# Kernel tuning notes

Hardware: AMD Instinct MI355X
Metric: run time of the kernel (lower is better)

## Reference

```python
import jax, jax.numpy as jnp
import numpy as np

NEG_INF = jnp.float32(-2**32 + 1)  # matches the module's padding constant


def setup_inputs() -> dict:
    key = jax.random.key(0)
    ks = jax.random.split(key, 20)
    T, N, E, R = 4, 20000, 320000, 2
    Din, Dh, H = 64, 64, 4
    s = 0.1  # xavier-ish scale
    inp = {
        "x": jax.random.normal(ks[0], (T, N, Din), jnp.float32),
        "edge_index": jax.random.randint(ks[1], (T, R, 2, E), 0, N, jnp.int32),
        "W_src": jax.random.normal(ks[2], (R, Din, H * Dh), jnp.float32) * s,
        "W_dst": jax.random.normal(ks[3], (R, Din, H * Dh), jnp.float32) * s,
        "att_src": jax.random.normal(ks[4], (R, H, Dh), jnp.float32) * s,
        "att_dst": jax.random.normal(ks[5], (R, H, Dh), jnp.float32) * s,
        "ra_W1": jax.random.normal(ks[6], (Dh, 4 * Dh), jnp.float32) * s,
        "ra_b1": jnp.zeros((4 * Dh,), jnp.float32),
        "ra_W2": jax.random.normal(ks[7], (4 * Dh, 1), jnp.float32) * s,
        "lstm_Wih": jax.random.normal(ks[8], (4 * Dh, Dh), jnp.float32) * s,
        "lstm_Whh": jax.random.normal(ks[9], (4 * Dh, Dh), jnp.float32) * s,
        "lstm_bih": jnp.zeros((4 * Dh,), jnp.float32),
        "lstm_bhh": jnp.zeros((4 * Dh,), jnp.float32),
        "pos_emb": jax.random.normal(ks[10], (T, Dh), jnp.float32) * s,
        "Wq": jax.random.normal(ks[11], (Dh, Dh), jnp.float32) * s,
        "Wk": jax.random.normal(ks[12], (Dh, Dh), jnp.float32) * s,
        "Wv": jax.random.normal(ks[13], (Dh, Dh), jnp.float32) * s,
    }
    return inp


def _gat(xt, ei, Ws, Wd, a_s, a_d, N, H, C):
    # PyG GATConv, concat=False, bias=False, eval mode (no dropout)
    src, dst = ei[0], ei[1]
    hs = (xt @ Ws).reshape(N, H, C)
    hd = (xt @ Wd).reshape(N, H, C)
    als = (hs * a_s[None]).sum(-1)          # [N,H]
    ald = (hd * a_d[None]).sum(-1)          # [N,H]
    e = jax.nn.leaky_relu(als[src] + ald[dst], 0.2)   # [E,H]
    m = jax.ops.segment_max(e, dst, num_segments=N)   # [N,H]
    p = jnp.exp(e - m[dst])
    denom = jax.ops.segment_sum(p, dst, num_segments=N)
    alpha = p / (denom[dst] + 1e-16)
    out = jax.ops.segment_sum(hs[src] * alpha[:, :, None], dst, num_segments=N)  # [N,H,C]
    return out.mean(1)                      # concat=False -> mean over heads


def reference(x, edge_index, W_src, W_dst, att_src, att_dst,
              ra_W1, ra_b1, ra_W2,
              lstm_Wih, lstm_Whh, lstm_bih, lstm_bhh,
              pos_emb, Wq, Wk, Wv):
    T, N, _ = x.shape
    R, H, C = att_src.shape   # C == n_hid (per-head GAT channels)

    # ---- intra-relation aggregation: GATConv per etype, vmapped over timeframes
    intra = []
    for r in range(R):
        f = jax.vmap(lambda xt, ei, r=r: _gat(xt, ei, W_src[r], W_dst[r],
                                              att_src[r], att_dst[r], N, H, C))
        intra.append(f(x, edge_index[:, r]))      # [T,N,C]
    h = jnp.stack(intra, axis=2)                  # [T,N,R,C]

    # ---- inter-relation aggregation (RelationAgg), batched over timeframes
    s = jnp.tanh(h @ ra_W1 + ra_b1) @ ra_W2       # [T,N,R,1]
    beta = jax.nn.softmax(s.mean(1), axis=1)      # mean over nodes, softmax over R -> [T,R,1]
    inter = (beta[:, None] * h).sum(2)            # [T,N,C]

    # ---- LSTM over time (batch = nodes)
    def step(carry, xt):
        hh, cc = carry
        g = xt @ lstm_Wih.T + hh @ lstm_Whh.T + lstm_bih + lstm_bhh
        i, f_, gg, o = jnp.split(g, 4, axis=-1)   # torch gate order i,f,g,o
        cc = jax.nn.sigmoid(f_) * cc + jax.nn.sigmoid(i) * jnp.tanh(gg)
        hh = jax.nn.sigmoid(o) * jnp.tanh(cc)
        return (hh, cc), hh
    z = jnp.zeros((N, C), x.dtype)
    _, hs_seq = jax.lax.scan(step, (z, z), inter)  # [T,N,C]
    feats = hs_seq.transpose(1, 0, 2)              # [N,T,C]

    # ---- temporal multi-head attention with causal mask, eval mode
    Ch = C // H
    ti = feats + pos_emb[None]                     # positions are just arange(T)
    qh = (ti @ Wq).reshape(N, T, H, Ch)
    kh = (ti @ Wk).reshape(N, T, H, Ch)
    vh = (ti @ Wv).reshape(N, T, H, Ch)
    scores = jnp.einsum('nqhc,nkhc->nhqk', qh, kh) / jnp.sqrt(jnp.float32(T))
    mask = jnp.tril(jnp.ones((T, T), bool))
    scores = jnp.where(mask[None, None], scores, NEG_INF)
    a = jax.nn.softmax(scores, axis=-1)
    out = jnp.einsum('nhqk,nkhc->nqhc', a, vh).reshape(N, T, C)
    return out  # output_features[ttype][ntype] == out[:, i, :]
```

## Files before the change

### kernel.cpp

```cpp
#include <hip/hip_runtime.h>
#include <hip/hip_bf16.h>

#define T_ 4
#define N_ 20000
#define E_ 320000
#define R_ 2
#define DIN 64
#define G_ 256
#define P_ 8
#define BPAD 18432
#define NB_ 32
#define EPB_ 10000
#define CHN_ 625

typedef unsigned short u16;
typedef __attribute__((ext_vector_type(8))) short bf16x8;
typedef __attribute__((ext_vector_type(2))) _Float16 h2;
typedef __attribute__((ext_vector_type(4))) float f32x4;

__device__ __forceinline__ float bf2f(u16 u) {
    unsigned int i = ((unsigned int)u) << 16; float f;
    __builtin_memcpy(&f, &i, 4); return f;
}
__device__ __forceinline__ u16 f2bf(float f) {
    unsigned int i; __builtin_memcpy(&i, &f, 4);
    unsigned int r = i + 0x7fffu + ((i >> 16) & 1u);
    return (u16)(r >> 16);
}
__device__ __forceinline__ u16 f2h(float f) {
    union { _Float16 h; u16 u; } c; c.h = (_Float16)f; return c.u;
}
__device__ __forceinline__ float sigm(float x) { return 1.f / (1.f + __expf(-x)); }
__device__ __forceinline__ float ftanh(float x) { return 1.f - 2.f / (__expf(2.f * x) + 1.f); }
__device__ __forceinline__ float fdot2(h2 a, h2 b, float c) {
#if __has_builtin(__builtin_amdgcn_fdot2)
    return __builtin_amdgcn_fdot2(a, b, c, false);
#else
    float r;
    asm("v_dot2_f32_f16 %0, %1, %2, %3" : "=v"(r) : "v"(a), "v"(b), "v"(c));
    return r;
#endif
}

__device__ __forceinline__ void gemm_direct(
    const u16* __restrict__ A, const u16* __restrict__ Bpad,
    int M, int Astride, int kchunks, int m0, f32x4* acc)
{
    const int tid = threadIdx.x;
    const int lane = tid & 63, wv = tid >> 6;
    const int col = lane & 15, quad = lane >> 4;
    #pragma unroll
    for (int cf = 0; cf < 16; ++cf) { acc[cf][0]=0.f; acc[cf][1]=0.f; acc[cf][2]=0.f; acc[cf][3]=0.f; }

    int row = m0 + wv * 16 + col;
    int row_c = (row < M) ? row : (M - 1);

    for (int kc = 0; kc < kchunks; ++kc) {
        #pragma unroll
        for (int ks = 0; ks < 2; ++ks) {
            bf16x8 a = *(const bf16x8*)(A + (size_t)row_c * Astride + kc * 64 + ks * 32 + quad * 8);
            const u16* bb = Bpad + kc * BPAD + ks * 32 + quad * 8;
            #pragma unroll
            for (int cf = 0; cf < 16; ++cf) {
                bf16x8 b = *(const bf16x8*)(bb + (cf * 16 + col) * 72);
                acc[cf] = __builtin_amdgcn_mfma_f32_16x16x32_bf16(a, b, acc[cf], 0, 0, 0);
            }
        }
    }
}

__global__ __launch_bounds__(256) void k_fold(
    const float* __restrict__ x, const float* __restrict__ wdall,
    float* __restrict__ als_all, float* __restrict__ ald_all, u16* __restrict__ x_h)
{
    __shared__ float wds[1024];
    {
        int tid = threadIdx.x;
        *(float4*)(wds + tid * 4) = *(const float4*)(wdall + tid * 4);
    }
    __syncthreads();

    int t = blockIdx.y;
    int idx = blockIdx.x * 256 + threadIdx.x;
    if (idx >= N_ * 4) return;
    int n = idx >> 2, q = idx & 3;
    const float* xr = x + ((size_t)t * N_ + n) * 64 + q * 16;
    float4 xv[4];
    #pragma unroll
    for (int i = 0; i < 4; ++i) xv[i] = *(const float4*)(xr + i * 4);

    {
        union { u16 h[16]; ushort4 s4[4]; } cv;
        #pragma unroll
        for (int i = 0; i < 4; ++i) {
            cv.h[i*4+0] = f2h(xv[i].x); cv.h[i*4+1] = f2h(xv[i].y);
            cv.h[i*4+2] = f2h(xv[i].z); cv.h[i*4+3] = f2h(xv[i].w);
        }
        u16* xo = x_h + ((size_t)t * N_ + n) * 64 + q * 16;
        #pragma unroll
        for (int i = 0; i < 4; ++i) *(ushort4*)(xo + i * 4) = cv.s4[i];
    }

    float s[16];
    #pragma unroll
    for (int i = 0; i < 16; ++i) s[i] = 0.f;
    #pragma unroll
    for (int i = 0; i < 4; ++i) {
        float xe[4] = {xv[i].x, xv[i].y, xv[i].z, xv[i].w};
        #pragma unroll
        for (int e = 0; e < 4; ++e) {
            int k = q * 16 + i * 4 + e;
            float xk = xe[e];
            #pragma unroll
            for (int tb = 0; tb < 4; ++tb) {
                float4 w = *(const float4*)(wds + tb * 256 + k * 4);
                s[tb*4+0] += xk * w.x; s[tb*4+1] += xk * w.y;
                s[tb*4+2] += xk * w.z; s[tb*4+3] += xk * w.w;
            }
        }
    }
    #pragma unroll
    for (int i = 0; i < 16; ++i) {
        s[i] += __shfl_xor(s[i], 1);
        s[i] += __shfl_xor(s[i], 2);
    }
    if (q == 0) {
        *(float4*)(als_all + ((size_t)(t*2+0) * N_ + n) * 4) = make_float4(s[0], s[1], s[2], s[3]);
        *(float4*)(als_all + ((size_t)(t*2+1) * N_ + n) * 4) = make_float4(s[4], s[5], s[6], s[7]);
        *(float4*)(ald_all + ((size_t)(t*2+0) * N_ + n) * 4) = make_float4(s[8], s[9], s[10], s[11]);
        *(float4*)(ald_all + ((size_t)(t*2+1) * N_ + n) * 4) = make_float4(s[12], s[13], s[14], s[15]);
    }
}

__global__ void k_prep(const float* __restrict__ Wdst, const float* __restrict__ att_dst,
                       const float* __restrict__ Wih, const float* __restrict__ Whh,
                       const float* __restrict__ bih, const float* __restrict__ bhh,
                       const float* __restrict__ Wsrc, const float* __restrict__ att_src,
                       const float* __restrict__ raW1,
                       const float* __restrict__ Wq, const float* __restrict__ Wk,
                       const float* __restrict__ Wv,
                       float* __restrict__ wdall, float* __restrict__ biasv,
                       u16* __restrict__ raW1_pad, u16* __restrict__ Wc_pad,
                       u16* __restrict__ qkv_pad, u16* __restrict__ postB_pad)
{
    int tid = threadIdx.x, bid = blockIdx.x;
    if (bid == 0) {
        int k = tid >> 2, h = tid & 3;
        for (int r = 0; r < 2; ++r) {
            float ss = 0.f, sd = 0.f;
            for (int c = 0; c < 64; ++c) {
                ss += Wsrc[((size_t)r * 64 + k) * 256 + h * 64 + c] * att_src[r * 256 + h * 64 + c];
                sd += Wdst[((size_t)r * 64 + k) * 256 + h * 64 + c] * att_dst[r * 256 + h * 64 + c];
            }
            wdall[r * 256 + k * 4 + h] = ss;
            wdall[512 + r * 256 + k * 4 + h] = sd;
        }
        biasv[tid] = bih[tid] + bhh[tid];
    }
    for (int i = bid * 256 + tid; i < BPAD; i += gridDim.x * 256) {
        int n = i / 72, kk = i % 72;
        raW1_pad[i] = (kk < 64) ? f2bf(raW1[kk * 256 + n]) : (u16)0;
    }
    for (int i = bid * 256 + tid; i < 2 * BPAD; i += gridDim.x * 256) {
        int kc = i / BPAD, q = i % BPAD, n = q / 72, kk = q % 72;
        const float* W = kc ? Whh : Wih;
        Wc_pad[i] = (kk < 64) ? f2bf(W[n * 64 + kk]) : (u16)0;
    }
    for (int i = bid * 256 + tid; i < 192 * 72; i += gridDim.x * 256) {
        int g = i / 72, kk = i % 72;
        int j = g >> 6, c = g & 63;
        const float* W = (j == 0) ? Wq : (j == 1) ? Wk : Wv;
        qkv_pad[i] = (kk < 64) ? f2bf(W[kk * 64 + c]) : (u16)0;
    }
    for (int i = bid * 256 + tid; i < 2 * 4 * 4608; i += gridDim.x * 256) {
        int r = i / 18432, q = i % 18432, kc = q / 4608, qq = q % 4608;
        int c = qq / 72, kk = qq % 72;
        postB_pad[i] = (kk < 64) ? f2bf(Wsrc[(size_t)r * 16384 + kk * 256 + kc * 64 + c]) : (u16)0;
    }
}

__global__ __launch_bounds__(256) void k_hist(const int* __restrict__ ei,
                                              u16* __restrict__ rank, u16* __restrict__ partial)
{
    __shared__ unsigned int hist[N_ / 2];
    int b = blockIdx.x, p = blockIdx.y, tid = threadIdx.x;
    for (int i = tid; i < N_ / 2; i += 256) hist[i] = 0u;
    __syncthreads();
    const int* dsts = ei + ((size_t)p * 2 + 1) * E_ + b * EPB_;
    u16* rk = rank + (size_t)p * E_ + b * EPB_;
    for (int e = tid; e < EPB_; e += 256) {
        int dst = dsts[e];
        unsigned sh = (unsigned)(dst & 1) * 16u;
        unsigned old = atomicAdd(&hist[dst >> 1], 1u << sh);
        rk[e] = (u16)((old >> sh) & 0xffffu);
    }
    __syncthreads();
    u16* part = partial + ((size_t)p * NB_ + b) * N_;
    for (int n = tid; n < N_; n += 256) {
        unsigned hv = hist[n >> 1];
        part[n] = (u16)((hv >> ((unsigned)(n & 1) * 16u)) & 0xffffu);
    }
}

__global__ __launch_bounds__(256) void k_scan1(u16* __restrict__ partial,
                                               int* __restrict__ offsets, int* __restrict__ chunktot)
{
    int p = blockIdx.y, ch = blockIdx.x;
    int tid = threadIdx.x, lane = tid & 63, wid = tid >> 6;
    __shared__ int wtot[4];
    u16* part = partial + (size_t)p * NB_ * N_;
    int* ofs = offsets + (size_t)p * (N_ + 1);
    int n0 = ch * CHN_;
    int carry = 0;
    for (int rnd = 0; rnd < 3; ++rnd) {
        int i = rnd * 256 + tid;
        int n = n0 + i;
        int v = 0;
        if (i < CHN_) {
            int run = 0;
            #pragma unroll 8
            for (int b = 0; b < NB_; ++b) {
                int pv = part[b * N_ + n];
                part[b * N_ + n] = (u16)run;
                run += pv;
            }
            v = run;
        }
        int incl = v;
        for (int d = 1; d < 64; d <<= 1) { int u = __shfl_up(incl, d); if (lane >= d) incl += u; }
        if (lane == 63) wtot[wid] = incl;
        __syncthreads();
        if (tid < 4) {
            int iv = wtot[tid];
            for (int d = 1; d < 4; d <<= 1) { int u = __shfl_up(iv, d); if (tid >= d) iv += u; }
            wtot[tid] = iv;
        }
        __syncthreads();
        int woff = (wid > 0) ? wtot[wid - 1] : 0;
        int tot = wtot[3];
        int excl = carry + woff + incl - v;
        if (i < CHN_) ofs[n] = excl;
        carry += tot;
        __syncthreads();
    }
    if (tid == 0) chunktot[p * NB_ + ch] = carry;
}

__global__ void k_scan2(const int* __restrict__ chunktot, int* __restrict__ chunkbase) {
    int tid = threadIdx.x;
    if (tid < P_) {
        int run = 0;
        for (int c = 0; c < NB_; ++c) {
            chunkbase[tid * NB_ + c] = run;
            run += chunktot[tid * NB_ + c];
        }
    }
}

__global__ void k_scan3(int* __restrict__ offsets, const int* __restrict__ chunkbase) {
    int p = blockIdx.y;
    int n = blockIdx.x * 256 + threadIdx.x;
    if (n < N_)
        offsets[(size_t)p * (N_ + 1) + n] += chunkbase[p * NB_ + n / CHN_];
    if (n == 0)
        offsets[(size_t)p * (N_ + 1) + N_] = E_;
}

__global__ void k_scatter(const int* __restrict__ ei, const int* __restrict__ offsets,
                          const u16* __restrict__ rank, const u16* __restrict__ partial,
                          u16* __restrict__ csr) {
    int bid = blockIdx.x;
    int p = bid & 7;
    int e = (bid >> 3) * 256 + threadIdx.x;
    int src = ei[((size_t)p * 2 + 0) * E_ + e];
    int dst = ei[((size_t)p * 2 + 1) * E_ + e];
    int b = e / EPB_;
    int pos = offsets[p * (N_ + 1) + dst]
            + (int)partial[((size_t)p * NB_ + b) * N_ + dst]
            + (int)rank[(size_t)p * E_ + e];
    csr[(size_t)p * E_ + pos] = (u16)src;
}

__global__ __launch_bounds__(256) void k_agg(
    const int* __restrict__ offsets, const u16* __restrict__ csr,
    const float* __restrict__ als_all, const float* __restrict__ ald_all,
    const u16* __restrict__ x_h, u16* __restrict__ xagg4)
{
    __shared__ __align__(16) u16 ptab[4][256];
    const int bid = blockIdx.x;
    const int p = bid & 7;
    const int t = p >> 1;
    const int* off   = offsets + (size_t)p * (N_ + 1);
    const u16* srcs  = csr + (size_t)p * E_;
    const float* als = als_all + (size_t)p * N_ * 4;
    const float* ald = ald_all + (size_t)p * N_ * 4;
    const u16* xb    = x_h + (size_t)t * N_ * 64;

    const int tid = threadIdx.x, lane = tid & 63, wv = tid >> 6;
    const int n = (bid >> 3) * 4 + wv;
    const int o0 = off[n], o1 = off[n + 1];
    const float4 aldv = *(const float4*)(ald + (size_t)n * 4);
    u16* pt = &ptab[wv][0];
    const int pw = (lane >> 1) * 8 + (lane & 1);

    float a0 = 0.f, a1 = 0.f, a2 = 0.f, a3 = 0.f;
    float d0 = 0.f, d1 = 0.f, d2 = 0.f, d3 = 0.f;

    for (int base = o0; base < o1; base += 64) {
        int cnt = o1 - base; if (cnt > 64) cnt = 64;
        int sv = 0;
        float p0 = 0.f, p1 = 0.f, p2 = 0.f, p3 = 0.f;
        if (lane < cnt) {
            sv = (int)srcs[base + lane];
            float4 av = *(const float4*)(als + (size_t)sv * 4);
            float e0 = av.x + aldv.x, e1 = av.y + aldv.y;
            float e2 = av.z + aldv.z, e3 = av.w + aldv.w;
            e0 = (e0 > 0.f) ? e0 : 0.2f * e0;
            e1 = (e1 > 0.f) ? e1 : 0.2f * e1;
            e2 = (e2 > 0.f) ? e2 : 0.2f * e2;
            e3 = (e3 > 0.f) ? e3 : 0.2f * e3;
            p0 = __expf(e0); p1 = __expf(e1); p2 = __expf(e2); p3 = __expf(e3);
        }
        d0 += p0; d1 += p1; d2 += p2; d3 += p3;
        pt[pw + 0] = f2h(p0); pt[pw + 2] = f2h(p1);
        pt[pw + 4] = f2h(p2); pt[pw + 6] = f2h(p3);
        int cntR = __builtin_amdgcn_readfirstlane((cnt + 7) & ~7);
        for (int j0 = 0; j0 < cntR; j0 += 8) {
            #pragma unroll
            for (int pr = 0; pr < 4; ++pr) {
                int j = j0 + pr * 2;
                int s0 = __builtin_amdgcn_readlane(sv, j);
                int s1 = __builtin_amdgcn_readlane(sv, j + 1);
                unsigned x0 = xb[((size_t)(unsigned)s0 << 6) + lane];
                unsigned x1 = xb[((size_t)(unsigned)s1 << 6) + lane];
                unsigned xp = x0 | (x1 << 16);
                uint4 pp = *(const uint4*)(pt + (j >> 1) * 8);
                h2 xv, q0, q1, q2, q3;
                __builtin_memcpy(&xv, &xp, 4);
                __builtin_memcpy(&q0, &pp.x, 4);
                __builtin_memcpy(&q1, &pp.y, 4);
                __builtin_memcpy(&q2, &pp.z, 4);
                __builtin_memcpy(&q3, &pp.w, 4);
                a0 = fdot2(xv, q0, a0);
                a1 = fdot2(xv, q1, a1);
                a2 = fdot2(xv, q2, a2);
                a3 = fdot2(xv, q3, a3);
            }
        }
    }
    #pragma unroll
    for (int m = 1; m < 64; m <<= 1) {
        d0 += __shfl_xor(d0, m); d1 += __shfl_xor(d1, m);
        d2 += __shfl_xor(d2, m); d3 += __shfl_xor(d3, m);
    }
    float s0 = 0.25f / (d0 + 1e-16f), s1 = 0.25f / (d1 + 1e-16f);
    float s2 = 0.25f / (d2 + 1e-16f), s3 = 0.25f / (d3 + 1e-16f);
    u16* outp = xagg4 + ((size_t)p * N_ + n) * 256 + lane;
    outp[0]   = f2bf(a0 * s0);
    outp[64]  = f2bf(a1 * s1);
    outp[128] = f2bf(a2 * s2);
    outp[192] = f2bf(a3 * s3);
}

__global__ __launch_bounds__(256) void k_post(
    const u16* __restrict__ xagg4, const u16* __restrict__ postB_pad,
    u16* __restrict__ intra)
{
    const int t = blockIdx.z, r = blockIdx.y;
    const u16* A = xagg4 + ((size_t)(t * 2 + r)) * N_ * 256;
    const u16* Bp = postB_pad + (size_t)r * 4 * 4608;
    const int tid = threadIdx.x, lane = tid & 63, wv = tid >> 6;
    const int col = lane & 15, quad = lane >> 4;
    int m0 = blockIdx.x * 64;
    int row = m0 + wv * 16 + col;
    int row_c = (row < N_) ? row : (N_ - 1);

    f32x4 acc[4];
    #pragma unroll
    for (int cf = 0; cf < 4; ++cf) { acc[cf][0]=0.f; acc[cf][1]=0.f; acc[cf][2]=0.f; acc[cf][3]=0.f; }
    #pragma unroll
    for (int kc = 0; kc < 4; ++kc) {
        #pragma unroll
        for (int ks = 0; ks < 2; ++ks) {
            bf16x8 a = *(const bf16x8*)(A + (size_t)row_c * 256 + kc * 64 + ks * 32 + quad * 8);
            const u16* bb = Bp + kc * 4608 + ks * 32 + quad * 8;
            #pragma unroll
            for (int cf = 0; cf < 4; ++cf) {
                bf16x8 b = *(const bf16x8*)(bb + (cf * 16 + col) * 72);
                acc[cf] = __builtin_amdgcn_mfma_f32_16x16x32_bf16(a, b, acc[cf], 0, 0, 0);
            }
        }
    }
    int rowbase = m0 + wv * 16 + quad * 4;
    #pragma unroll
    for (int cf = 0; cf < 4; ++cf) {
        int c = cf * 16 + col;
        #pragma unroll
        for (int reg = 0; reg < 4; ++reg) {
            int rr = rowbase + reg;
            if (rr < N_)
                intra[(((size_t)t * N_ + rr) * 2 + r) * 64 + c] = f2bf(acc[cf][reg]);
        }
    }
}

__global__ __launch_bounds__(256) void k_relagg(
    const u16* __restrict__ A, const u16* __restrict__ W1pad, const float* __restrict__ b1,
    const float* __restrict__ W2, float* __restrict__ ssum)
{
    int m0 = blockIdx.x * 64;
    f32x4 acc[16];
    gemm_direct(A, W1pad, T_ * N_ * R_, 64, 1, m0, acc);

    const int tid = threadIdx.x, lane = tid & 63, wv = tid >> 6;
    const int col = lane & 15;
    float sp[4] = {0.f, 0.f, 0.f, 0.f};
    #pragma unroll
    for (int cf = 0; cf < 16; ++cf) {
        int gcol = cf * 16 + col;
        float bb = b1[gcol];
        float ww = W2[gcol];
        #pragma unroll
        for (int reg = 0; reg < 4; ++reg)
            sp[reg] += ftanh(acc[cf][reg] + bb) * ww;
    }
    #pragma unroll
    for (int reg = 0; reg < 4; ++reg) {
        float v = sp[reg];
        v += __shfl_xor(v, 1); v += __shfl_xor(v, 2);
        v += __shfl_xor(v, 4); v += __shfl_xor(v, 8);
        sp[reg] = v;
    }
    float se = sp[0] + sp[2];
    float so = sp[1] + sp[3];
    se += __shfl_xor(se, 16); se += __shfl_xor(se, 32);
    so += __shfl_xor(so, 16); so += __shfl_xor(so, 32);
    __shared__ float red[8];
    if (lane == 0) { red[wv * 2] = se; red[wv * 2 + 1] = so; }
    __syncthreads();
    if (tid == 0) {
        float s0 = red[0] + red[2] + red[4] + red[6];
        float s1 = red[1] + red[3] + red[5] + red[7];
        int t = m0 / (N_ * R_);
        atomicAdd(&ssum[t * 2 + 0], s0);
        atomicAdd(&ssum[t * 2 + 1], s1);
    }
}

__global__ __launch_bounds__(256) void k_lstm(
    const u16* __restrict__ intra, const float* __restrict__ ssum,
    const u16* __restrict__ Wc_pad, const float* __restrict__ biasv,
    u16* __restrict__ feats)
{
    __shared__ __align__(16) u16 hl[64][72];
    const int tid = threadIdx.x, lane = tid & 63, wv = tid >> 6;
    const int col = lane & 15, quad = lane >> 4;
    int m0 = blockIdx.x * 64;
    int row = m0 + wv * 16 + col;
    int row_c = (row < N_) ? row : (N_ - 1);
    int rowbase = m0 + wv * 16 + quad * 4;

    float betas[8];
    #pragma unroll
    for (int t = 0; t < 4; ++t) {
        float s0 = ssum[t * 2] * (1.f / N_), s1 = ssum[t * 2 + 1] * (1.f / N_);
        float mx = fmaxf(s0, s1);
        float e0 = __expf(s0 - mx), e1 = __expf(s1 - mx);
        float inv = 1.f / (e0 + e1);
        betas[t * 2] = e0 * inv; betas[t * 2 + 1] = e1 * inv;
    }

    float cc[4][4];
    #pragma unroll
    for (int j = 0; j < 4; ++j)
        #pragma unroll
        for (int reg = 0; reg < 4; ++reg) cc[j][reg] = 0.f;

    for (int t = 0; t < 4; ++t) {
        float b0 = betas[t * 2], b1 = betas[t * 2 + 1];
        const u16* ib = intra + ((size_t)t * N_ + row_c) * 128;

        f32x4 acc[16];
        #pragma unroll
        for (int cf = 0; cf < 16; ++cf) { acc[cf][0]=0.f; acc[cf][1]=0.f; acc[cf][2]=0.f; acc[cf][3]=0.f; }

        #pragma unroll
        for (int ks = 0; ks < 2; ++ks) {
            int coff = ks * 32 + quad * 8;
            bf16x8 i0 = *(const bf16x8*)(ib + coff);
            bf16x8 i1 = *(const bf16x8*)(ib + 64 + coff);
            union { u16 h[8]; bf16x8 v; } cv;
            #pragma unroll
            for (int j = 0; j < 8; ++j)
                cv.h[j] = f2bf(b0 * bf2f((u16)i0[j]) + b1 * bf2f((u16)i1[j]));
            const u16* bb = Wc_pad + ks * 32 + quad * 8;
            #pragma unroll
            for (int cf = 0; cf < 16; ++cf) {
                bf16x8 b = *(const bf16x8*)(bb + (cf * 16 + col) * 72);
                acc[cf] = __builtin_amdgcn_mfma_f32_16x16x32_bf16(cv.v, b, acc[cf], 0, 0, 0);
            }
        }
        if (t > 0) {
            #pragma unroll
            for (int ks = 0; ks < 2; ++ks) {
                bf16x8 a = *(const bf16x8*)&hl[wv * 16 + col][ks * 32 + quad * 8];
                const u16* bb = Wc_pad + BPAD + ks * 32 + quad * 8;
                #pragma unroll
                for (int cf = 0; cf < 16; ++cf) {
                    bf16x8 b = *(const bf16x8*)(bb + (cf * 16 + col) * 72);
                    acc[cf] = __builtin_amdgcn_mfma_f32_16x16x32_bf16(a, b, acc[cf], 0, 0, 0);
                }
            }
        }

        #pragma unroll
        for (int j = 0; j < 4; ++j) {
            int c = j * 16 + col;
            float bi = biasv[c], bf_ = biasv[64 + c], bg = biasv[128 + c], bo = biasv[192 + c];
            #pragma unroll
            for (int reg = 0; reg < 4; ++reg) {
                float gi = acc[j][reg] + bi;
                float gf = acc[j + 4][reg] + bf_;
                float gg = acc[j + 8][reg] + bg;
                float go = acc[j + 12][reg] + bo;
                float c2 = sigm(gf) * cc[j][reg] + sigm(gi) * ftanh(gg);
                float hh = sigm(go) * ftanh(c2);
                cc[j][reg] = c2;
                u16 hb = f2bf(hh);
                hl[wv * 16 + quad * 4 + reg][c] = hb;
                int rr = rowbase + reg;
                if (rr < N_)
                    feats[(size_t)rr * 256 + t * 64 + c] = hb;
            }
        }
    }
}

__global__ __launch_bounds__(256) void k_attn(
    const u16* __restrict__ feats, const float* __restrict__ pos_emb,
    const u16* __restrict__ qkv_pad, float* __restrict__ out)
{
    __shared__ float qkv_s[64 * 200];
    const int tid = threadIdx.x, lane = tid & 63, wv = tid >> 6;
    const int col = lane & 15, quad = lane >> 4;
    int m0 = blockIdx.x * 64;
    int row = m0 + wv * 16 + col;
    int trow = row & 3;

    f32x4 acc[12];
    #pragma unroll
    for (int cf = 0; cf < 12; ++cf) { acc[cf][0]=0.f; acc[cf][1]=0.f; acc[cf][2]=0.f; acc[cf][3]=0.f; }
    #pragma unroll
    for (int ks = 0; ks < 2; ++ks) {
        int coff = ks * 32 + quad * 8;
        bf16x8 fv = *(const bf16x8*)(feats + (size_t)row * 64 + coff);
        float4 p0 = *(const float4*)(pos_emb + trow * 64 + coff);
        float4 p1 = *(const float4*)(pos_emb + trow * 64 + coff + 4);
        union { u16 h[8]; bf16x8 v; } cv;
        cv.h[0] = f2bf(bf2f((u16)fv[0]) + p0.x); cv.h[1] = f2bf(bf2f((u16)fv[1]) + p0.y);
        cv.h[2] = f2bf(bf2f((u16)fv[2]) + p0.z); cv.h[3] = f2bf(bf2f((u16)fv[3]) + p0.w);
        cv.h[4] = f2bf(bf2f((u16)fv[4]) + p1.x); cv.h[5] = f2bf(bf2f((u16)fv[5]) + p1.y);
        cv.h[6] = f2bf(bf2f((u16)fv[6]) + p1.z); cv.h[7] = f2bf(bf2f((u16)fv[7]) + p1.w);
        bf16x8 a = cv.v;
        const u16* bb = qkv_pad + ks * 32 + quad * 8;
        #pragma unroll
        for (int cf = 0; cf < 12; ++cf) {
            bf16x8 b = *(const bf16x8*)(bb + (cf * 16 + col) * 72);
            acc[cf] = __builtin_amdgcn_mfma_f32_16x16x32_bf16(a, b, acc[cf], 0, 0, 0);
        }
    }
    #pragma unroll
    for (int cf = 0; cf < 12; ++cf) {
        int g = cf * 16 + col;
        #pragma unroll
        for (int reg = 0; reg < 4; ++reg) {
            int rl = wv * 16 + quad * 4 + reg;
            qkv_s[rl * 200 + g] = acc[cf][reg];
        }
    }
    __syncthreads();

    int nl = wv * 4 + (lane >> 4);
    int sub = lane & 15;
    int h = sub >> 2, tq = sub & 3;
    const float* qrow = qkv_s + (nl * 4 + tq) * 200 + h * 16;

    float s[4];
    #pragma unroll
    for (int tk = 0; tk < 4; ++tk) {
        const float* krow = qkv_s + (nl * 4 + tk) * 200 + 64 + h * 16;
        float d = 0.f;
        #pragma unroll
        for (int j = 0; j < 16; ++j) d += qrow[j] * krow[j];
        s[tk] = (tk > tq) ? -4294967295.0f : d * 0.5f;
    }
    float mx = fmaxf(fmaxf(s[0], s[1]), fmaxf(s[2], s[3]));
    float a0 = __expf(s[0]-mx), a1 = __expf(s[1]-mx), a2 = __expf(s[2]-mx), a3 = __expf(s[3]-mx);
    float inv = 1.f / (a0 + a1 + a2 + a3);
    a0 *= inv; a1 *= inv; a2 *= inv; a3 *= inv;

    int n = blockIdx.x * 16 + nl;
    const float* v0 = qkv_s + (nl * 4 + 0) * 200 + 128 + h * 16;
    const float* v1 = v0 + 200, *v2 = v0 + 400, *v3 = v0 + 600;
    #pragma unroll
    for (int cc4 = 0; cc4 < 4; ++cc4) {
        float4 o;
        o.x = a0*v0[cc4*4+0] + a1*v1[cc4*4+0] + a2*v2[cc4*4+0] + a3*v3[cc4*4+0];
        o.y = a0*v0[cc4*4+1] + a1*v1[cc4*4+1] + a2*v2[cc4*4+1] + a3*v3[cc4*4+1];
        o.z = a0*v0[cc4*4+2] + a1*v1[cc4*4+2] + a2*v2[cc4*4+2] + a3*v3[cc4*4+2];
        o.w = a0*v0[cc4*4+3] + a1*v1[cc4*4+3] + a2*v2[cc4*4+3] + a3*v3[cc4*4+3];
        *(float4*)(out + (size_t)n * 256 + tq * 64 + h * 16 + cc4 * 4) = o;
    }
}

extern "C" void kernel_launch(void* const* d_in, const int* in_sizes, int n_in,
                              void* d_out, int out_size, void* d_ws, size_t ws_size,
                              hipStream_t stream) {
    const float* x     = (const float*)d_in[0];
    const int* ei      = (const int*)d_in[1];
    const float* Wsrc  = (const float*)d_in[2];
    const float* Wdst  = (const float*)d_in[3];
    const float* att_src = (const float*)d_in[4];
    const float* att_dst = (const float*)d_in[5];
    const float* raW1  = (const float*)d_in[6];
    const float* rab1  = (const float*)d_in[7];
    const float* raW2  = (const float*)d_in[8];
    const float* Wih   = (const float*)d_in[9];
    const float* Whh   = (const float*)d_in[10];
    const float* bih   = (const float*)d_in[11];
    const float* bhh   = (const float*)d_in[12];
    const float* pos   = (const float*)d_in[13];
    const float* Wq    = (const float*)d_in[14];
    const float* Wk    = (const float*)d_in[15];
    const float* Wv    = (const float*)d_in[16];
    float* out = (float*)d_out;

    char* w = (char*)d_ws;
    size_t off = 0;
    auto alloc = [&](size_t bytes) -> char* {
        char* pp = w + off; off += (bytes + 255) & ~(size_t)255; return pp;
    };
    u16*   intra     = (u16*)  alloc((size_t)T_ * N_ * R_ * 64 * 2);
    u16*   x_h       = (u16*)  alloc((size_t)T_ * N_ * 64 * 2);
    float* ssum      = (float*)alloc(256);
    float* wdall     = (float*)alloc(1024 * 4);
    float* biasv     = (float*)alloc(256 * 4);
    u16*   raW1_pad  = (u16*)  alloc(BPAD * 2);
    u16*   Wc_pad    = (u16*)  alloc(2 * BPAD * 2);
    u16*   qkv_pad   = (u16*)  alloc(192 * 72 * 2);
    u16*   postB_pad = (u16*)  alloc(2 * 4 * 4608 * 2);
    int*   chunktot  = (int*)  alloc(P_ * NB_ * 4);
    int*   chunkbase = (int*)  alloc(P_ * NB_ * 4);
    char*  ubase   = alloc(0);
    size_t uoff = 0;
    auto ualloc = [&](size_t bytes) -> char* {
        char* pp = ubase + uoff; uoff += (bytes + 255) & ~(size_t)255; return pp;
    };
    int*   offsets = (int*)  ualloc((size_t)P_ * (N_ + 1) * 4);
    u16*   csr     = (u16*)  ualloc((size_t)P_ * E_ * 2);
    float* als_all = (float*)ualloc((size_t)P_ * N_ * 4 * 4);
    float* ald_all = (float*)ualloc((size_t)P_ * N_ * 4 * 4);
    u16*   partial = (u16*)  ualloc((size_t)P_ * NB_ * N_ * 2);
    u16*   xagg4   = (u16*)  ualloc((size_t)P_ * N_ * 256 * 2);
    u16*   rank    = (u16*)  xagg4;
    u16*   feats   = (u16*)  ubase;
    (void)ws_size; (void)in_sizes; (void)n_in; (void)out_size;

    k_prep<<<72, 256, 0, stream>>>(Wdst, att_dst, Wih, Whh, bih, bhh, Wsrc, att_src, raW1,
                                   Wq, Wk, Wv, wdall, biasv, raW1_pad, Wc_pad, qkv_pad, postB_pad);
    k_hist<<<dim3(NB_, 8), 256, 0, stream>>>(ei, rank, partial);
    k_scan1<<<dim3(NB_, 8), 256, 0, stream>>>(partial, offsets, chunktot);
    k_scan2<<<1, 64, 0, stream>>>(chunktot, chunkbase);
    k_scan3<<<dim3(79, 8), 256, 0, stream>>>(offsets, chunkbase);
    k_scatter<<<10000, 256, 0, stream>>>(ei, offsets, rank, partial, csr);
    k_fold<<<dim3(313, 4), 256, 0, stream>>>(x, wdall, als_all, ald_all, x_h);
    k_agg<<<40000, 256, 0, stream>>>(offsets, csr, als_all, ald_all, x_h, xagg4);
    k_post<<<dim3(313, 2, 4), 256, 0, stream>>>(xagg4, postB_pad, intra);
    hipMemsetAsync(ssum, 0, 32, stream);
    k_relagg<<<2500, 256, 0, stream>>>(intra, raW1_pad, rab1, raW2, ssum);
    k_lstm<<<313, 256, 0, stream>>>(intra, ssum, Wc_pad, biasv, feats);
    k_attn<<<1250, 256, 0, stream>>>(feats, pos, qkv_pad, out);
}
```

Measured before the change: 461.9 us.

## Process four destination nodes per wave in GAT aggregation and fuse scan kernels

The aggregation kernel now assigns four destination nodes to each wavefront, with 16 lanes computing edge softmax weights per node instead of 64 lanes for one node. Average degree is about 16, so the old layout left most lanes idle during weight computation. Each wave keeps four accumulator sets, reduces the denominators within 16-lane groups and packs the bf16 outputs with a single convert instruction. The tiny single-block k_scan2 is merged into k_scan3 through a wave-level shuffle scan, which removes one launch. In exchange, nodes with uneven degrees in the same wave cause divergence, and register pressure goes up.

```diff
diff --git a/kernel.cpp b/kernel.cpp
--- a/kernel.cpp
+++ b/kernel.cpp
@@ -32,6 +32,11 @@
 }
 __device__ __forceinline__ float sigm(float x) { return 1.f / (1.f + __expf(-x)); }
 __device__ __forceinline__ float ftanh(float x) { return 1.f - 2.f / (__expf(2.f * x) + 1.f); }
+__device__ __forceinline__ float rdlanef(float v, int l) {
+    int i; __builtin_memcpy(&i, &v, 4);
+    int r = __builtin_amdgcn_readlane(i, l);
+    float f; __builtin_memcpy(&f, &r, 4); return f;
+}
 __device__ __forceinline__ float fdot2(h2 a, h2 b, float c) {
 #if __has_builtin(__builtin_amdgcn_fdot2)
     return __builtin_amdgcn_fdot2(a, b, c, false);
@@ -40,6 +45,11 @@
     asm("v_dot2_f32_f16 %0, %1, %2, %3" : "=v"(r) : "v"(a), "v"(b), "v"(c));
     return r;
 #endif
+}
+__device__ __forceinline__ unsigned cvtpk_bf16(float lo, float hi) {
+    unsigned r;
+    asm("v_cvt_pk_bf16_f32 %0, %1, %2" : "=v"(r) : "v"(lo), "v"(hi));
+    return r;
 }
 
 __device__ __forceinline__ void gemm_direct(
@@ -246,22 +256,23 @@
     if (tid == 0) chunktot[p * NB_ + ch] = carry;
 }
 
-__global__ void k_scan2(const int* __restrict__ chunktot, int* __restrict__ chunkbase) {
+__global__ void k_scan3(int* __restrict__ offsets, const int* __restrict__ chunktot) {
+    __shared__ int cb[NB_];
+    int p = blockIdx.y;
     int tid = threadIdx.x;
-    if (tid < P_) {
-        int run = 0;
-        for (int c = 0; c < NB_; ++c) {
-            chunkbase[tid * NB_ + c] = run;
-            run += chunktot[tid * NB_ + c];
-        }
-    }
-}
-
-__global__ void k_scan3(int* __restrict__ offsets, const int* __restrict__ chunkbase) {
-    int p = blockIdx.y;
-    int n = blockIdx.x * 256 + threadIdx.x;
-    if (n < N_)
-        offsets[(size_t)p * (N_ + 1) + n] += chunkbase[p * NB_ + n / CHN_];
+    if (tid < 64) {
+        int v = (tid < NB_) ? chunktot[p * NB_ + tid] : 0;
+        #pragma unroll
+        for (int d = 1; d < NB_; d <<= 1) { int u = __shfl_up(v, d); if (tid >= d) v += u; }
+        if (tid < NB_) cb[tid] = v;
+    }
+    __syncthreads();
+    int n = blockIdx.x * 256 + tid;
+    if (n < N_) {
+        int c = n / CHN_;
+        int base = (c > 0) ? cb[c - 1] : 0;
+        offsets[(size_t)p * (N_ + 1) + n] += base;
+    }
     if (n == 0)
         offsets[(size_t)p * (N_ + 1) + N_] = E_;
 }
@@ -286,7 +297,7 @@
     const float* __restrict__ als_all, const float* __restrict__ ald_all,
     const u16* __restrict__ x_h, u16* __restrict__ xagg4)
 {
-    __shared__ __align__(16) u16 ptab[4][256];
+    __shared__ __align__(16) u16 ptab[4][4][64];
     const int bid = blockIdx.x;
     const int p = bid & 7;
     const int t = p >> 1;
@@ -297,69 +308,90 @@
     const u16* xb    = x_h + (size_t)t * N_ * 64;
 
     const int tid = threadIdx.x, lane = tid & 63, wv = tid >> 6;
-    const int n = (bid >> 3) * 4 + wv;
-    const int o0 = off[n], o1 = off[n + 1];
-    const float4 aldv = *(const float4*)(ald + (size_t)n * 4);
-    u16* pt = &ptab[wv][0];
-    const int pw = (lane >> 1) * 8 + (lane & 1);
-
-    float a0 = 0.f, a1 = 0.f, a2 = 0.f, a3 = 0.f;
+    const int g = lane >> 4, el = lane & 15;
+    const int n0 = (bid >> 3) * 16 + wv * 4;
+    const int ng = n0 + g;
+    const int o0 = off[ng], o1 = off[ng + 1];
+    const int deg = o1 - o0;
+    const float4 aldv = *(const float4*)(ald + (size_t)ng * 4);
+    u16* pt = &ptab[wv][0][0];
+    const int pw = g * 64 + (el >> 1) * 8 + (el & 1);
+
+    int sdeg[4];
+    #pragma unroll
+    for (int q = 0; q < 4; ++q) sdeg[q] = __builtin_amdgcn_readlane(deg, q * 16);
+    int mdeg = max(max(sdeg[0], sdeg[1]), max(sdeg[2], sdeg[3]));
+    int nrounds = (mdeg + 15) >> 4;
+
+    float acc[4][4];
+    #pragma unroll
+    for (int q = 0; q < 4; ++q)
+        #pragma unroll
+        for (int h = 0; h < 4; ++h) acc[q][h] = 0.f;
     float d0 = 0.f, d1 = 0.f, d2 = 0.f, d3 = 0.f;
 
-    for (int base = o0; base < o1; base += 64) {
-        int cnt = o1 - base; if (cnt > 64) cnt = 64;
+    for (int rr = 0; rr < nrounds; ++rr) {
+        int e = rr * 16 + el;
         int sv = 0;
         float p0 = 0.f, p1 = 0.f, p2 = 0.f, p3 = 0.f;
-        if (lane < cnt) {
-            sv = (int)srcs[base + lane];
+        if (e < deg) {
+            sv = (int)srcs[o0 + e];
             float4 av = *(const float4*)(als + (size_t)sv * 4);
             float e0 = av.x + aldv.x, e1 = av.y + aldv.y;
             float e2 = av.z + aldv.z, e3 = av.w + aldv.w;
-            e0 = (e0 > 0.f) ? e0 : 0.2f * e0;
-            e1 = (e1 > 0.f) ? e1 : 0.2f * e1;
-            e2 = (e2 > 0.f) ? e2 : 0.2f * e2;
-            e3 = (e3 > 0.f) ? e3 : 0.2f * e3;
+            e0 = fmaxf(e0, 0.2f * e0); e1 = fmaxf(e1, 0.2f * e1);
+            e2 = fmaxf(e2, 0.2f * e2); e3 = fmaxf(e3, 0.2f * e3);
             p0 = __expf(e0); p1 = __expf(e1); p2 = __expf(e2); p3 = __expf(e3);
         }
         d0 += p0; d1 += p1; d2 += p2; d3 += p3;
         pt[pw + 0] = f2h(p0); pt[pw + 2] = f2h(p1);
         pt[pw + 4] = f2h(p2); pt[pw + 6] = f2h(p3);
-        int cntR = __builtin_amdgcn_readfirstlane((cnt + 7) & ~7);
-        for (int j0 = 0; j0 < cntR; j0 += 8) {
-            #pragma unroll
-            for (int pr = 0; pr < 4; ++pr) {
-                int j = j0 + pr * 2;
-                int s0 = __builtin_amdgcn_readlane(sv, j);
-                int s1 = __builtin_amdgcn_readlane(sv, j + 1);
-                unsigned x0 = xb[((size_t)(unsigned)s0 << 6) + lane];
-                unsigned x1 = xb[((size_t)(unsigned)s1 << 6) + lane];
-                unsigned xp = x0 | (x1 << 16);
-                uint4 pp = *(const uint4*)(pt + (j >> 1) * 8);
-                h2 xv, q0, q1, q2, q3;
-                __builtin_memcpy(&xv, &xp, 4);
-                __builtin_memcpy(&q0, &pp.x, 4);
-                __builtin_memcpy(&q1, &pp.y, 4);
-                __builtin_memcpy(&q2, &pp.z, 4);
-                __builtin_memcpy(&q3, &pp.w, 4);
-                a0 = fdot2(xv, q0, a0);
-                a1 = fdot2(xv, q1, a1);
-                a2 = fdot2(xv, q2, a2);
-                a3 = fdot2(xv, q3, a3);
-            }
-        }
-    }
-    #pragma unroll
-    for (int m = 1; m < 64; m <<= 1) {
-        d0 += __shfl_xor(d0, m); d1 += __shfl_xor(d1, m);
-        d2 += __shfl_xor(d2, m); d3 += __shfl_xor(d3, m);
-    }
-    float s0 = 0.25f / (d0 + 1e-16f), s1 = 0.25f / (d1 + 1e-16f);
-    float s2 = 0.25f / (d2 + 1e-16f), s3 = 0.25f / (d3 + 1e-16f);
-    u16* outp = xagg4 + ((size_t)p * N_ + n) * 256 + lane;
-    outp[0]   = f2bf(a0 * s0);
-    outp[64]  = f2bf(a1 * s1);
-    outp[128] = f2bf(a2 * s2);
-    outp[192] = f2bf(a3 * s3);
+        #pragma unroll
+        for (int q = 0; q < 4; ++q) {
+            if (sdeg[q] > rr * 16) {
+                const u16* ptq = pt + q * 64;
+                #pragma unroll
+                for (int pr = 0; pr < 8; ++pr) {
+                    int s0i = __builtin_amdgcn_readlane(sv, q * 16 + pr * 2);
+                    int s1i = __builtin_amdgcn_readlane(sv, q * 16 + pr * 2 + 1);
+                    unsigned x0 = xb[((size_t)(unsigned)s0i << 6) + lane];
+                    unsigned x1 = xb[((size_t)(unsigned)s1i << 6) + lane];
+                    unsigned xp = x0 | (x1 << 16);
+                    uint4 ppv = *(const uint4*)(ptq + pr * 8);
+                    h2 xv, q0, q1, q2, q3;
+                    __builtin_memcpy(&xv, &xp, 4);
+                    __builtin_memcpy(&q0, &ppv.x, 4);
+                    __builtin_memcpy(&q1, &ppv.y, 4);
+                    __builtin_memcpy(&q2, &ppv.z, 4);
+                    __builtin_memcpy(&q3, &ppv.w, 4);
+                    acc[q][0] = fdot2(xv, q0, acc[q][0]);
+                    acc[q][1] = fdot2(xv, q1, acc[q][1]);
+                    acc[q][2] = fdot2(xv, q2, acc[q][2]);
+                    acc[q][3] = fdot2(xv, q3, acc[q][3]);
+                }
+            }
+        }
+    }
+    d0 += __shfl_xor(d0, 1); d0 += __shfl_xor(d0, 2);
+    d0 += __shfl_xor(d0, 4); d0 += __shfl_xor(d0, 8);
+    d1 += __shfl_xor(d1, 1); d1 += __shfl_xor(d1, 2);
+    d1 += __shfl_xor(d1, 4); d1 += __shfl_xor(d1, 8);
+    d2 += __shfl_xor(d2, 1); d2 += __shfl_xor(d2, 2);
+    d2 += __shfl_xor(d2, 4); d2 += __shfl_xor(d2, 8);
+    d3 += __shfl_xor(d3, 1); d3 += __shfl_xor(d3, 2);
+    d3 += __shfl_xor(d3, 4); d3 += __shfl_xor(d3, 8);
+    #pragma unroll
+    for (int q = 0; q < 4; ++q) {
+        float s0 = 0.25f / (rdlanef(d0, q * 16) + 1e-16f);
+        float s1 = 0.25f / (rdlanef(d1, q * 16) + 1e-16f);
+        float s2 = 0.25f / (rdlanef(d2, q * 16) + 1e-16f);
+        float s3 = 0.25f / (rdlanef(d3, q * 16) + 1e-16f);
+        unsigned w01 = cvtpk_bf16(acc[q][0] * s0, acc[q][1] * s1);
+        unsigned w23 = cvtpk_bf16(acc[q][2] * s2, acc[q][3] * s3);
+        u16* outp = xagg4 + ((size_t)p * N_ + n0 + q) * 256 + lane;
+        outp[0]   = (u16)w01;  outp[64]  = (u16)(w01 >> 16);
+        outp[128] = (u16)w23;  outp[192] = (u16)(w23 >> 16);
+    }
 }
 
 __global__ __launch_bounds__(256) void k_post(
@@ -650,7 +682,6 @@
     u16*   qkv_pad   = (u16*)  alloc(192 * 72 * 2);
     u16*   postB_pad = (u16*)  alloc(2 * 4 * 4608 * 2);
     int*   chunktot  = (int*)  alloc(P_ * NB_ * 4);
-    int*   chunkbase = (int*)  alloc(P_ * NB_ * 4);
     char*  ubase   = alloc(0);
     size_t uoff = 0;
     auto ualloc = [&](size_t bytes) -> char* {
@@ -670,11 +701,10 @@
                                    Wq, Wk, Wv, wdall, biasv, raW1_pad, Wc_pad, qkv_pad, postB_pad);
     k_hist<<<dim3(NB_, 8), 256, 0, stream>>>(ei, rank, partial);
     k_scan1<<<dim3(NB_, 8), 256, 0, stream>>>(partial, offsets, chunktot);
-    k_scan2<<<1, 64, 0, stream>>>(chunktot, chunkbase);
-    k_scan3<<<dim3(79, 8), 256, 0, stream>>>(offsets, chunkbase);
+    k_scan3<<<dim3(79, 8), 256, 0, stream>>>(offsets, chunktot);
     k_scatter<<<10000, 256, 0, stream>>>(ei, offsets, rank, partial, csr);
     k_fold<<<dim3(313, 4), 256, 0, stream>>>(x, wdall, als_all, ald_all, x_h);
-    k_agg<<<40000, 256, 0, stream>>>(offsets, csr, als_all, ald_all, x_h, xagg4);
+    k_agg<<<10000, 256, 0, stream>>>(offsets, csr, als_all, ald_all, x_h, xagg4);
     k_post<<<dim3(313, 2, 4), 256, 0, stream>>>(xagg4, postB_pad, intra);
     hipMemsetAsync(ssum, 0, 32, stream);
     k_relagg<<<2500, 256, 0, stream>>>(intra, raW1_pad, rab1, raW2, ssum);
```

After: 450.8 us. -2.4%, faster.
